# Optimization experiments

Hardware: AMD Instinct MI355X
Metric: run time of the kernel (lower is better)

## Reference

```python
import jax, jax.numpy as jnp
import numpy as np

N_NODES = 12800
N_EDGES = 204800
DIM = 16
EDGE_DIM = 4
NUM_FEAT = 3


def setup_inputs() -> dict:
    key = jax.random.key(0)
    ks = jax.random.split(key, 16)
    s = 0.1
    return {
        "x": jax.random.normal(ks[0], (N_NODES, NUM_FEAT), jnp.float32),
        "edge_index": jax.random.randint(ks[1], (2, N_EDGES), 0, N_NODES, jnp.int32),
        "edge_attr": jax.random.uniform(ks[2], (N_EDGES, EDGE_DIM), jnp.float32),
        "lin0_w": jax.random.normal(ks[3], (DIM, NUM_FEAT), jnp.float32) * s,
        "lin0_b": jax.random.normal(ks[4], (DIM,), jnp.float32) * s,
        "nn1_w": jax.random.normal(ks[5], (DIM, EDGE_DIM), jnp.float32) * s,
        "nn1_b": jax.random.normal(ks[6], (DIM,), jnp.float32) * s,
        "nn2_w": jax.random.normal(ks[7], (DIM * DIM, DIM), jnp.float32) * s,
        "nn2_b": jax.random.normal(ks[8], (DIM * DIM,), jnp.float32) * s,
        "conv_root": jax.random.normal(ks[9], (DIM, DIM), jnp.float32) * s,
        "conv_bias": jax.random.normal(ks[10], (DIM,), jnp.float32) * s,
        "gru_w_ih": jax.random.normal(ks[11], (3 * DIM, DIM), jnp.float32) * s,
        "gru_w_hh": jax.random.normal(ks[12], (3 * DIM, DIM), jnp.float32) * s,
        "gru_b_ih": jax.random.normal(ks[13], (3 * DIM,), jnp.float32) * s,
        "gru_b_hh": jax.random.normal(ks[14], (3 * DIM,), jnp.float32) * s,
    }


def _forward(x, edge_index, edge_attr, lin0_w, lin0_b, nn1_w, nn1_b, nn2_w, nn2_b,
             conv_root, conv_bias, gru_w_ih, gru_w_hh, gru_b_ih, gru_b_hh):
    n = x.shape[0]
    dim = lin0_w.shape[0]
    src, dst = edge_index[0], edge_index[1]

    # edge-conditioned weight matrices, shared across the 6 rounds: [E, dim, dim]
    e_hidden = jax.nn.relu(edge_attr @ nn1_w.T + nn1_b)
    edge_w = (e_hidden @ nn2_w.T + nn2_b).reshape(-1, dim, dim)

    # in-degree for mean aggregation (0 -> divide by 1, result stays 0)
    deg = jax.ops.segment_sum(jnp.ones_like(dst, dtype=x.dtype), dst, num_segments=n)
    inv_deg = (1.0 / jnp.maximum(deg, 1.0))[:, None]

    out = jax.nn.relu(x @ lin0_w.T + lin0_b)  # [N, dim]
    h = out
    for _ in range(6):
        # gather -> per-edge matmul -> scatter-mean
        msg = jnp.einsum('ed,edk->ek', out[src], edge_w)  # [E, dim]
        aggr = jax.ops.segment_sum(msg, dst, num_segments=n) * inv_deg
        m = jax.nn.relu(aggr + out @ conv_root + conv_bias)
        # single GRU step (seq_len = 1)
        gi = m @ gru_w_ih.T + gru_b_ih  # [N, 3*dim]
        gh = h @ gru_w_hh.T + gru_b_hh
        i_r, i_z, i_n = jnp.split(gi, 3, axis=-1)
        h_r, h_z, h_n = jnp.split(gh, 3, axis=-1)
        r = jax.nn.sigmoid(i_r + h_r)
        z = jax.nn.sigmoid(i_z + h_z)
        nhat = jnp.tanh(i_n + r * h_n)
        h = (1.0 - z) * nhat + z * h
        out = h
    return out


def reference(x, edge_index, edge_attr, lin0_w, lin0_b, nn1_w, nn1_b, nn2_w, nn2_b,
              conv_root, conv_bias, gru_w_ih, gru_w_hh, gru_b_ih, gru_b_hh):
    return _forward(x, edge_index, edge_attr, lin0_w, lin0_b, nn1_w, nn1_b, nn2_w,
                    nn2_b, conv_root, conv_bias, gru_w_ih, gru_w_hh, gru_b_ih, gru_b_hh)
```

## Files before the change

### kernel.cpp

```cpp
#include <hip/hip_runtime.h>

#define NN 12800
#define NE 204800
#define BCAP 64

#define OFF_W2 0
#define OFF_CR 4416
#define OFF_WI 4736
#define OFF_WH 5696
#define OFF_CB 6656
#define OFF_BI 6672
#define OFF_BH 6720
#define PACKN  6768

__device__ __align__(16) float g_outA[NN * 16];
__device__ __align__(16) float g_outB[NN * 16];
__device__ __align__(16) float g_ehsB[NN * BCAP * 16];
__device__ __align__(16) int g_srcB[NN * BCAP];
__device__ int g_cnt[NN];
__device__ __align__(16) float g_wpack[PACKN];

__global__ __launch_bounds__(256) void k_setup(const int* __restrict__ ei,
                                               const float* __restrict__ x,
                                               const float* __restrict__ lw,
                                               const float* __restrict__ lb,
                                               const float* __restrict__ attr,
                                               const float* __restrict__ w1,
                                               const float* __restrict__ b1,
                                               const float* __restrict__ nn2_w,
                                               const float* __restrict__ nn2_b,
                                               const float* __restrict__ cr,
                                               const float* __restrict__ cb,
                                               const float* __restrict__ wi,
                                               const float* __restrict__ wh,
                                               const float* __restrict__ bi,
                                               const float* __restrict__ bh) {
    int gid = blockIdx.x * 256 + threadIdx.x;

    if (blockIdx.x == 0) {
        int tt = threadIdx.x;
        for (int i = tt; i < 4096; i += 256)
            g_wpack[OFF_W2 + (i & 15) * 276 + ((i >> 4) & 15) * 16 + (i >> 8)] = nn2_w[i];
        g_wpack[OFF_W2 + (tt >> 4) * 276 + 256 + (tt & 15)] = nn2_b[tt];
        g_wpack[OFF_CR + (tt & 15) * 20 + (tt >> 4)] = cr[tt];
        for (int i = tt; i < 768; i += 256) {
            g_wpack[OFF_WI + (i >> 4) * 20 + (i & 15)] = wi[i];
            g_wpack[OFF_WH + (i >> 4) * 20 + (i & 15)] = wh[i];
        }
        if (tt < 16) g_wpack[OFF_CB + tt] = cb[tt];
        if (tt < 48) { g_wpack[OFF_BI + tt] = bi[tt]; g_wpack[OFF_BH + tt] = bh[tt]; }
    }

    if (gid < NN) {
        int n = gid;
        float x0 = x[n * 3 + 0], x1 = x[n * 3 + 1], x2 = x[n * 3 + 2];
        float v[16];
#pragma unroll
        for (int j = 0; j < 16; ++j) {
            float t = lb[j] + x0 * lw[j * 3 + 0] + x1 * lw[j * 3 + 1] + x2 * lw[j * 3 + 2];
            v[j] = fmaxf(t, 0.0f);
        }
#pragma unroll
        for (int j = 0; j < 16; j += 4)
            *(float4*)(g_outA + n * 16 + j) = make_float4(v[j], v[j + 1], v[j + 2], v[j + 3]);
    }

    int e = gid;
    int s = ei[e], d = ei[NE + e];
    float4 a = *(const float4*)(attr + e * 4);
    float v[16];
#pragma unroll
    for (int j = 0; j < 16; ++j) {
        float t = b1[j] + a.x * w1[j * 4 + 0] + a.y * w1[j * 4 + 1] +
                  a.z * w1[j * 4 + 2] + a.w * w1[j * 4 + 3];
        v[j] = fmaxf(t, 0.0f);
    }
    int pos = atomicAdd(&g_cnt[d], 1);
    if (pos < BCAP) {
        int slot = d * BCAP + pos;
        g_srcB[slot] = s;
#pragma unroll
        for (int j = 0; j < 16; j += 4)
            *(float4*)(g_ehsB + slot * 16 + j) = make_float4(v[j], v[j + 1], v[j + 2], v[j + 3]);
    }
}

__global__ __launch_bounds__(256) void k_round(float* __restrict__ out_final,
                                               int flip, int last) {
    __shared__ __align__(16) float s_pack[PACKN];
    int t = threadIdx.x;
    {
        const float4* srcp = (const float4*)g_wpack;
        float4* dstp = (float4*)s_pack;
#pragma unroll
        for (int i = 0; i < PACKN / 4 / 256 + 1; ++i) {
            int idx = t + i * 256;
            if (idx < PACKN / 4) dstp[idx] = srcp[idx];
        }
    }
    __syncthreads();

    const float* s_W2  = s_pack + OFF_W2;
    const float* s_crT = s_pack + OFF_CR;
    const float* s_wi  = s_pack + OFF_WI;
    const float* s_wh  = s_pack + OFF_WH;
    const float* s_cb  = s_pack + OFF_CB;
    const float* s_bi  = s_pack + OFF_BI;
    const float* s_bh  = s_pack + OFF_BH;

    const float* cur = flip ? g_outB : g_outA;
    float*       nxt = flip ? g_outA : g_outB;

    const int grp = t >> 4, j = t & 15;
    const int n = blockIdx.x * 16 + grp;
    int deg = min(g_cnt[n], BCAP);
    if (last && j == 0) g_cnt[n] = 0;
    const int base = n * BCAP;

    float Gd[16];
#pragma unroll
    for (int d = 0; d < 16; ++d) Gd[d] = 0.0f;
    float r16 = 0.0f;
#pragma unroll 4
    for (int q = 0; q < deg; ++q) {
        int slot = base + q;
        int s = min(g_srcB[slot], NN - 1);
        const float* orow = cur + s * 16;
        float ej = g_ehsB[slot * 16 + j];
        float4 o0 = *(const float4*)(orow + 0);
        float4 o1 = *(const float4*)(orow + 4);
        float4 o2 = *(const float4*)(orow + 8);
        float4 o3 = *(const float4*)(orow + 12);
        Gd[0]  += ej * o0.x; Gd[1]  += ej * o0.y; Gd[2]  += ej * o0.z; Gd[3]  += ej * o0.w;
        Gd[4]  += ej * o1.x; Gd[5]  += ej * o1.y; Gd[6]  += ej * o1.z; Gd[7]  += ej * o1.w;
        Gd[8]  += ej * o2.x; Gd[9]  += ej * o2.y; Gd[10] += ej * o2.z; Gd[11] += ej * o2.w;
        Gd[12] += ej * o3.x; Gd[13] += ej * o3.y; Gd[14] += ej * o3.z; Gd[15] += ej * o3.w;
        r16 += orow[j];
    }

    const float* wj = s_W2 + j * 276;
    float part[16];
#pragma unroll
    for (int kp = 0; kp < 16; ++kp) {
        const float* w = wj + kp * 16;
        float4 w0 = *(const float4*)(w + 0);
        float4 w1 = *(const float4*)(w + 4);
        float4 w2 = *(const float4*)(w + 8);
        float4 w3 = *(const float4*)(w + 12);
        part[kp] = Gd[0] * w0.x + Gd[1] * w0.y + Gd[2] * w0.z + Gd[3] * w0.w
                 + Gd[4] * w1.x + Gd[5] * w1.y + Gd[6] * w1.z + Gd[7] * w1.w
                 + Gd[8] * w2.x + Gd[9] * w2.y + Gd[10] * w2.z + Gd[11] * w2.w
                 + Gd[12] * w3.x + Gd[13] * w3.y + Gd[14] * w3.z + Gd[15] * w3.w;
    }
    {
        float4 b0 = *(const float4*)(wj + 256);
        float4 b1 = *(const float4*)(wj + 260);
        float4 b2v = *(const float4*)(wj + 264);
        float4 b3 = *(const float4*)(wj + 268);
        part[0] += r16 * b0.x;  part[1] += r16 * b0.y;  part[2] += r16 * b0.z;  part[3] += r16 * b0.w;
        part[4] += r16 * b1.x;  part[5] += r16 * b1.y;  part[6] += r16 * b1.z;  part[7] += r16 * b1.w;
        part[8] += r16 * b2v.x; part[9] += r16 * b2v.y; part[10] += r16 * b2v.z; part[11] += r16 * b2v.w;
        part[12] += r16 * b3.x; part[13] += r16 * b3.y; part[14] += r16 * b3.z; part[15] += r16 * b3.w;
    }

    float w8[8];
#pragma unroll
    for (int i = 0; i < 8; ++i) {
        int keep = 2 * i + (j & 1);
        w8[i] = part[keep] + __shfl_xor(part[keep ^ 1], 1);
    }
    float w4[4];
#pragma unroll
    for (int i = 0; i < 4; ++i) {
        int keep = 2 * i + ((j >> 1) & 1);
        w4[i] = w8[keep] + __shfl_xor(w8[keep ^ 1], 2);
    }
    float w2[2];
#pragma unroll
    for (int i = 0; i < 2; ++i) {
        int keep = 2 * i + ((j >> 2) & 1);
        w2[i] = w4[keep] + __shfl_xor(w4[keep ^ 1], 4);
    }
    float aggr;
    {
        int keep = (j >> 3) & 1;
        aggr = w2[keep] + __shfl_xor(w2[keep ^ 1], 8);
    }
    float invd = 1.0f / (float)(deg > 0 ? deg : 1);
    float a_k = aggr * invd;
    const int k = j;

    const float* nrow = cur + n * 16;
    float4 q0 = *(const float4*)(nrow + 0);
    float4 q1 = *(const float4*)(nrow + 4);
    float4 q2 = *(const float4*)(nrow + 8);
    float4 q3 = *(const float4*)(nrow + 12);
    float o[16] = {q0.x, q0.y, q0.z, q0.w, q1.x, q1.y, q1.z, q1.w,
                   q2.x, q2.y, q2.z, q2.w, q3.x, q3.y, q3.z, q3.w};
    float ok = o[k];

    float mcc = s_cb[k] + a_k;
    {
        const float* c = s_crT + k * 20;
        float4 c0 = *(const float4*)(c + 0);
        float4 c1 = *(const float4*)(c + 4);
        float4 c2 = *(const float4*)(c + 8);
        float4 c3 = *(const float4*)(c + 12);
        mcc += o[0] * c0.x + o[1] * c0.y + o[2] * c0.z + o[3] * c0.w
             + o[4] * c1.x + o[5] * c1.y + o[6] * c1.z + o[7] * c1.w
             + o[8] * c2.x + o[9] * c2.y + o[10] * c2.z + o[11] * c2.w
             + o[12] * c3.x + o[13] * c3.y + o[14] * c3.z + o[15] * c3.w;
    }
    float m = fmaxf(mcc, 0.0f);

    float md[16];
#pragma unroll
    for (int d = 0; d < 16; ++d) md[d] = __shfl(m, d, 16);

    float ir = s_bi[k], iz = s_bi[16 + k], in_ = s_bi[32 + k];
    float hr = s_bh[k], hz = s_bh[16 + k], hh = s_bh[32 + k];
#pragma unroll
    for (int g = 0; g < 3; ++g) {
        const float* wrow_i = s_wi + (g * 16 + k) * 20;
        const float* wrow_h = s_wh + (g * 16 + k) * 20;
        float acc_i = 0.0f, acc_h = 0.0f;
#pragma unroll
        for (int d4 = 0; d4 < 4; ++d4) {
            float4 wiv = *(const float4*)(wrow_i + d4 * 4);
            float4 whv = *(const float4*)(wrow_h + d4 * 4);
            acc_i += md[d4 * 4] * wiv.x + md[d4 * 4 + 1] * wiv.y
                   + md[d4 * 4 + 2] * wiv.z + md[d4 * 4 + 3] * wiv.w;
            acc_h += o[d4 * 4] * whv.x + o[d4 * 4 + 1] * whv.y
                   + o[d4 * 4 + 2] * whv.z + o[d4 * 4 + 3] * whv.w;
        }
        if (g == 0) { ir += acc_i; hr += acc_h; }
        else if (g == 1) { iz += acc_i; hz += acc_h; }
        else { in_ += acc_i; hh += acc_h; }
    }
    float rg = 1.0f / (1.0f + __expf(-(ir + hr)));
    float z  = 1.0f / (1.0f + __expf(-(iz + hz)));
    float nh = tanhf(in_ + rg * hh);
    float hnew = (1.0f - z) * nh + z * ok;

    if (last) out_final[n * 16 + k] = hnew;
    else      nxt[n * 16 + k] = hnew;
}

extern "C" void kernel_launch(void* const* d_in, const int* in_sizes, int n_in,
                              void* d_out, int out_size, void* d_ws, size_t ws_size,
                              hipStream_t stream) {
    const float* x         = (const float*)d_in[0];
    const int*   ei        = (const int*)d_in[1];
    const float* edge_attr = (const float*)d_in[2];
    const float* lin0_w    = (const float*)d_in[3];
    const float* lin0_b    = (const float*)d_in[4];
    const float* nn1_w     = (const float*)d_in[5];
    const float* nn1_b     = (const float*)d_in[6];
    const float* nn2_w     = (const float*)d_in[7];
    const float* nn2_b     = (const float*)d_in[8];
    const float* conv_root = (const float*)d_in[9];
    const float* conv_bias = (const float*)d_in[10];
    const float* gru_w_ih  = (const float*)d_in[11];
    const float* gru_w_hh  = (const float*)d_in[12];
    const float* gru_b_ih  = (const float*)d_in[13];
    const float* gru_b_hh  = (const float*)d_in[14];
    float* out = (float*)d_out;

    k_setup<<<NE / 256, 256, 0, stream>>>(ei, x, lin0_w, lin0_b, edge_attr,
                                          nn1_w, nn1_b, nn2_w, nn2_b, conv_root,
                                          conv_bias, gru_w_ih, gru_w_hh,
                                          gru_b_ih, gru_b_hh);

    for (int r = 0; r < 6; ++r) {
        k_round<<<NN / 16, 256, 0, stream>>>(out, r & 1, r == 5 ? 1 : 0);
    }
}
```

Before: 249.1 us.

## Store edge hidden features as paired fp16 and process edges two at a time

Per-edge hidden features (16 floats per edge) are now stored as fp16, interleaved so that two consecutive edges of a node share one __half2 per channel. The gather loop processes edge pairs, loading both source indices with one int2 read and both edge values with one half2 read, and handles an odd remainder separately. This halves the bytes read for edge features on each of the six rounds and raises memory-level parallelism per iteration. The cost is reduced precision of the edge hidden activations, plus scattered 2-byte stores in setup.

After: 265.4 us. 6.5% more time.

```diff
diff --git a/kernel.cpp b/kernel.cpp
--- a/kernel.cpp
+++ b/kernel.cpp
@@ -1,4 +1,5 @@
 #include <hip/hip_runtime.h>
+#include <hip/hip_fp16.h>
 
 #define NN 12800
 #define NE 204800
@@ -15,7 +16,7 @@
 
 __device__ __align__(16) float g_outA[NN * 16];
 __device__ __align__(16) float g_outB[NN * 16];
-__device__ __align__(16) float g_ehsB[NN * BCAP * 16];
+__device__ __align__(16) __half2 g_ehsP[NN * 32 * 16];
 __device__ __align__(16) int g_srcB[NN * BCAP];
 __device__ int g_cnt[NN];
 __device__ __align__(16) float g_wpack[PACKN];
@@ -77,11 +78,13 @@
     }
     int pos = atomicAdd(&g_cnt[d], 1);
     if (pos < BCAP) {
-        int slot = d * BCAP + pos;
-        g_srcB[slot] = s;
-#pragma unroll
-        for (int j = 0; j < 16; j += 4)
-            *(float4*)(g_ehsB + slot * 16 + j) = make_float4(v[j], v[j + 1], v[j + 2], v[j + 3]);
+        g_srcB[d * BCAP + pos] = s;
+        int pair = pos >> 1, par = pos & 1;
+        __half* hp = (__half*)g_ehsP;
+        int hbase = ((d * 32 + pair) * 16) * 2 + par;
+#pragma unroll
+        for (int j = 0; j < 16; ++j)
+            hp[hbase + j * 2] = __float2half(v[j]);
     }
 }
 
@@ -116,17 +119,47 @@
     int deg = min(g_cnt[n], BCAP);
     if (last && j == 0) g_cnt[n] = 0;
     const int base = n * BCAP;
+    const __half2* ehp = g_ehsP + n * 512;
 
     float Gd[16];
 #pragma unroll
     for (int d = 0; d < 16; ++d) Gd[d] = 0.0f;
     float r16 = 0.0f;
-#pragma unroll 4
-    for (int q = 0; q < deg; ++q) {
-        int slot = base + q;
-        int s = min(g_srcB[slot], NN - 1);
+
+    const int npair = deg >> 1;
+#pragma unroll 2
+    for (int p = 0; p < npair; ++p) {
+        int2 ss = *(const int2*)(g_srcB + base + 2 * p);
+        __half2 e2 = ehp[p * 16 + j];
+        float ej0 = __low2float(e2);
+        float ej1 = __high2float(e2);
+        int s0 = min(ss.x, NN - 1);
+        int s1 = min(ss.y, NN - 1);
+        const float* orow0 = cur + s0 * 16;
+        const float* orow1 = cur + s1 * 16;
+        float4 a0 = *(const float4*)(orow0 + 0);
+        float4 a1 = *(const float4*)(orow0 + 4);
+        float4 a2 = *(const float4*)(orow0 + 8);
+        float4 a3 = *(const float4*)(orow0 + 12);
+        float4 b0 = *(const float4*)(orow1 + 0);
+        float4 b1 = *(const float4*)(orow1 + 4);
+        float4 b2 = *(const float4*)(orow1 + 8);
+        float4 b3 = *(const float4*)(orow1 + 12);
+        Gd[0]  += ej0 * a0.x + ej1 * b0.x; Gd[1]  += ej0 * a0.y + ej1 * b0.y;
+        Gd[2]  += ej0 * a0.z + ej1 * b0.z; Gd[3]  += ej0 * a0.w + ej1 * b0.w;
+        Gd[4]  += ej0 * a1.x + ej1 * b1.x; Gd[5]  += ej0 * a1.y + ej1 * b1.y;
+        Gd[6]  += ej0 * a1.z + ej1 * b1.z; Gd[7]  += ej0 * a1.w + ej1 * b1.w;
+        Gd[8]  += ej0 * a2.x + ej1 * b2.x; Gd[9]  += ej0 * a2.y + ej1 * b2.y;
+        Gd[10] += ej0 * a2.z + ej1 * b2.z; Gd[11] += ej0 * a2.w + ej1 * b2.w;
+        Gd[12] += ej0 * a3.x + ej1 * b3.x; Gd[13] += ej0 * a3.y + ej1 * b3.y;
+        Gd[14] += ej0 * a3.z + ej1 * b3.z; Gd[15] += ej0 * a3.w + ej1 * b3.w;
+        r16 += orow0[j] + orow1[j];
+    }
+    if (deg & 1) {
+        int q = deg - 1;
+        int s = min(g_srcB[base + q], NN - 1);
         const float* orow = cur + s * 16;
-        float ej = g_ehsB[slot * 16 + j];
+        float ej = __low2float(ehp[(q >> 1) * 16 + j]);
         float4 o0 = *(const float4*)(orow + 0);
         float4 o1 = *(const float4*)(orow + 4);
         float4 o2 = *(const float4*)(orow + 8);
```

## Fuse six round kernels into one persistent cooperative kernel with grid barrier

Applied to the files above, without the earlier changes.

Replaces the six per-round launches with one cooperative persistent kernel of 256 blocks of 1024 threads. Each thread group handles one node and a sense-reversing global barrier separates the rounds. This removes five kernel launch gaps and five reloads of the weight pack into shared memory. In exchange it adds global atomic barrier cost, and 1024-thread blocks may lower occupancy and latency hiding for the gather-heavy loop. The old per-round launches remain as a fallback if the cooperative launch fails.

Measured after the change: 553.8 us. 2.22x slower.

```diff
diff --git a/kernel.cpp b/kernel.cpp
--- a/kernel.cpp
+++ b/kernel.cpp
@@ -3,6 +3,7 @@
 #define NN 12800
 #define NE 204800
 #define BCAP 64
+#define PBLK 256
 
 #define OFF_W2 0
 #define OFF_CR 4416
@@ -19,6 +20,32 @@
 __device__ __align__(16) int g_srcB[NN * BCAP];
 __device__ int g_cnt[NN];
 __device__ __align__(16) float g_wpack[PACKN];
+
+__device__ int g_bar_cnt   = 0;
+__device__ int g_bar_sense = 0;
+
+__device__ __forceinline__ void gbar(int* sense) {
+    __syncthreads();
+    if (threadIdx.x == 0) {
+        int s = *sense ^ 1;
+        *sense = s;
+        __threadfence();
+        int a = __hip_atomic_fetch_add(&g_bar_cnt, 1, __ATOMIC_ACQ_REL,
+                                       __HIP_MEMORY_SCOPE_AGENT);
+        if (a == PBLK - 1) {
+            __hip_atomic_store(&g_bar_cnt, 0, __ATOMIC_RELAXED,
+                               __HIP_MEMORY_SCOPE_AGENT);
+            __hip_atomic_store(&g_bar_sense, s, __ATOMIC_RELEASE,
+                               __HIP_MEMORY_SCOPE_AGENT);
+        } else {
+            while (__hip_atomic_load(&g_bar_sense, __ATOMIC_ACQUIRE,
+                                     __HIP_MEMORY_SCOPE_AGENT) != s)
+                __builtin_amdgcn_s_sleep(16);
+        }
+        __threadfence();
+    }
+    __syncthreads();
+}
 
 __global__ __launch_bounds__(256) void k_setup(const int* __restrict__ ei,
                                                const float* __restrict__ x,
@@ -85,21 +112,9 @@
     }
 }
 
-__global__ __launch_bounds__(256) void k_round(float* __restrict__ out_final,
-                                               int flip, int last) {
-    __shared__ __align__(16) float s_pack[PACKN];
-    int t = threadIdx.x;
-    {
-        const float4* srcp = (const float4*)g_wpack;
-        float4* dstp = (float4*)s_pack;
-#pragma unroll
-        for (int i = 0; i < PACKN / 4 / 256 + 1; ++i) {
-            int idx = t + i * 256;
-            if (idx < PACKN / 4) dstp[idx] = srcp[idx];
-        }
-    }
-    __syncthreads();
-
+__device__ __forceinline__ void round_body(const float* s_pack, int n, int j,
+                                           const float* cur, float* nxt,
+                                           float* out_final, int last) {
     const float* s_W2  = s_pack + OFF_W2;
     const float* s_crT = s_pack + OFF_CR;
     const float* s_wi  = s_pack + OFF_WI;
@@ -108,11 +123,6 @@
     const float* s_bi  = s_pack + OFF_BI;
     const float* s_bh  = s_pack + OFF_BH;
 
-    const float* cur = flip ? g_outB : g_outA;
-    float*       nxt = flip ? g_outA : g_outB;
-
-    const int grp = t >> 4, j = t & 15;
-    const int n = blockIdx.x * 16 + grp;
     int deg = min(g_cnt[n], BCAP);
     if (last && j == 0) g_cnt[n] = 0;
     const int base = n * BCAP;
@@ -244,6 +254,49 @@
 
     if (last) out_final[n * 16 + k] = hnew;
     else      nxt[n * 16 + k] = hnew;
+}
+
+__global__ __launch_bounds__(1024) void k_persist(float* __restrict__ out_final) {
+    __shared__ __align__(16) float s_pack[PACKN];
+    int t = threadIdx.x;
+    {
+        const float4* srcp = (const float4*)g_wpack;
+        float4* dstp = (float4*)s_pack;
+        for (int idx = t; idx < PACKN / 4; idx += 1024) dstp[idx] = srcp[idx];
+    }
+    __syncthreads();
+
+    int sense = 0;
+    const int g = blockIdx.x * 64 + (t >> 4);
+    const int j = t & 15;
+
+    for (int r = 0; r < 6; ++r) {
+        const float* cur = (r & 1) ? g_outB : g_outA;
+        float*       nxt = (r & 1) ? g_outA : g_outB;
+        if (g < NN)
+            round_body(s_pack, g, j, cur, nxt, out_final, r == 5 ? 1 : 0);
+        gbar(&sense);
+    }
+}
+
+__global__ __launch_bounds__(256) void k_round(float* __restrict__ out_final,
+                                               int flip, int last) {
+    __shared__ __align__(16) float s_pack[PACKN];
+    int t = threadIdx.x;
+    {
+        const float4* srcp = (const float4*)g_wpack;
+        float4* dstp = (float4*)s_pack;
+#pragma unroll
+        for (int i = 0; i < PACKN / 4 / 256 + 1; ++i) {
+            int idx = t + i * 256;
+            if (idx < PACKN / 4) dstp[idx] = srcp[idx];
+        }
+    }
+    __syncthreads();
+    const float* cur = flip ? g_outB : g_outA;
+    float*       nxt = flip ? g_outA : g_outB;
+    int n = blockIdx.x * 16 + (t >> 4);
+    round_body(s_pack, n, t & 15, cur, nxt, out_final, last);
 }
 
 extern "C" void kernel_launch(void* const* d_in, const int* in_sizes, int n_in,
@@ -271,7 +324,12 @@
                                           conv_bias, gru_w_ih, gru_w_hh,
                                           gru_b_ih, gru_b_hh);
 
-    for (int r = 0; r < 6; ++r) {
-        k_round<<<NN / 16, 256, 0, stream>>>(out, r & 1, r == 5 ? 1 : 0);
-    }
-}
+    void* args[] = { (void*)&out };
+    hipError_t err = hipLaunchCooperativeKernel((const void*)k_persist,
+                                                dim3(PBLK), dim3(1024),
+                                                args, 0, stream);
+    if (err != hipSuccess) {
+        for (int r = 0; r < 6; ++r)
+            k_round<<<NN / 16, 256, 0, stream>>>(out, r & 1, r == 5 ? 1 : 0);
+    }
+}
```
